# Kernel tuning notes

Measured on AMD Instinct MI355X. Metric: run time of the kernel, lower is better.

## Reference

```python
import jax, jax.numpy as jnp
import numpy as np


def _build_kkt(A, B, x0, C, c, T):
    n_state, n_ctrl = B.shape
    n_all = n_state + n_ctrl
    N = n_all * T          # primal dim (z)
    M = n_state * T        # dual dim (mu)
    dt = A.dtype

    # TL = block_diag(C_0, ..., C_{T-1})  -> [N, N]
    t = jnp.arange(T)
    ra = jnp.arange(n_all)
    rows = t[:, None, None] * n_all + ra[None, :, None]
    cols = t[:, None, None] * n_all + ra[None, None, :]
    TL = jnp.zeros((N, N), dt).at[rows, cols].set(C)

    # BL = dynamics constraint matrix  -> [M, N]
    AB = jnp.concatenate([A, B], axis=1)            # [n_state, n_all]
    BL = jnp.zeros((M, N), dt)
    BL = BL.at[:n_state, :n_state].set(jnp.eye(n_state, dtype=dt))
    ti = jnp.arange(T - 1)
    rs = jnp.arange(n_state)
    # AB blocks: rows n_state + i*n_state, cols i*n_all (i = 0..T-2)
    br = (ti[:, None, None] + 1) * n_state + rs[None, :, None]
    bc = ti[:, None, None] * n_all + ra[None, None, :]
    BL = BL.at[br, bc].set(jnp.broadcast_to(AB, (T - 1, n_state, n_all)))
    # -1 identity blocks: BL[n_state*t + i, n_all*t + i] = -1 for t = 1..T-1
    BL = BL.at[(ti[:, None] + 1) * n_state + rs[None, :],
               (ti[:, None] + 1) * n_all + rs[None, :]].set(-1.0)

    Full = jnp.block([[TL, BL.T],
                      [BL, jnp.zeros((M, M), dt)]])
    b = jnp.zeros(M, dt).at[:n_state].set(x0)
    sol = jnp.concatenate([-c.reshape(-1), b])
    return Full, sol, N


def setup_inputs() -> dict:
    key = jax.random.key(0)
    kA, kB, kx, kC, kc = jax.random.split(key, 5)
    T, n_state, n_ctrl = 128, 16, 8
    n_all = n_state + n_ctrl
    A = 0.3 * jax.random.normal(kA, (n_state, n_state), jnp.float32)
    B = 0.3 * jax.random.normal(kB, (n_state, n_ctrl), jnp.float32)
    x0 = jax.random.normal(kx, (n_state,), jnp.float32)
    Mrand = 0.1 * jax.random.normal(kC, (T, n_all, n_all), jnp.float32)
    C = jnp.eye(n_all, dtype=jnp.float32)[None] + jnp.einsum('tij,tkj->tik', Mrand, Mrand)
    c = jax.random.normal(kc, (T, n_all), jnp.float32)
    return {"A": A, "B": B, "x0": x0, "C": C, "c": c, "T": T}


def reference(A, B, x0, C, c, T):
    Full, sol, N = _build_kkt(A, B, x0, C, c, T)
    mu_z = jnp.linalg.solve(Full, sol)
    z, mu = mu_z[:N], mu_z[N:]
    return (z, mu)
```

## Files before the change

### kernel.cpp

```cpp
#include <hip/hip_runtime.h>


constexpr int T  = 128;
constexpr int NA = 24;

__device__ __forceinline__ float dot16r(const float* lds, const float* r, float s) {
    const float4* a4 = (const float4*)lds;
#pragma unroll
    for (int q = 0; q < 4; ++q) {
        float4 x = a4[q];
        s = fmaf(x.x, r[4 * q + 0], s); s = fmaf(x.y, r[4 * q + 1], s);
        s = fmaf(x.z, r[4 * q + 2], s); s = fmaf(x.w, r[4 * q + 3], s);
    }
    return s;
}
__device__ __forceinline__ float dot16f4(const float* a, const float* b, float s) {
    const float4* a4 = (const float4*)a;
    const float4* b4 = (const float4*)b;
#pragma unroll
    for (int q = 0; q < 4; ++q) {
        float4 x = a4[q], y = b4[q];
        s = fmaf(x.x, y.x, s); s = fmaf(x.y, y.y, s);
        s = fmaf(x.z, y.z, s); s = fmaf(x.w, y.w, s);
    }
    return s;
}

__global__ __launch_bounds__(256, 1)
void lqr_solve(const float* __restrict__ gA,
               const float* __restrict__ gB,
               const float* __restrict__ gx0,
               const float* __restrict__ gC,
               const float* __restrict__ gc,
               float* __restrict__ out,
               float* __restrict__ Pws,
               float* __restrict__ pws,
               float* __restrict__ Fws,
               float* __restrict__ dws)
{
    __shared__ __align__(16) float A_sh[16][16];
    __shared__ __align__(16) float At_sh[16][16];
    __shared__ __align__(16) float B_sh[16][8];
    __shared__ __align__(16) float Bt_sh[8][16];
    __shared__ __align__(16) float P_sh[2][16][20];
    __shared__ __align__(16) float p_sh[2][16];
    __shared__ __align__(16) float Wt[16][20];
    __shared__ __align__(16) float Vt[8][20];
    __shared__ __align__(16) float Gu[16][8];
    __shared__ __align__(16) float Aug[2][8][27];
    __shared__ __align__(16) float Kall[T][8][16];
    __shared__ __align__(16) float kall[T][8];
    __shared__ __align__(16) float c_sh[T][NA];
    __shared__ __align__(16) float z_sh[T][NA];
    __shared__ __align__(16) float Csh[2][24][25];

    const int tid = threadIdx.x;

    {
        const int i = tid >> 4, j = tid & 15;
        const float v = gA[tid];
        A_sh[i][j] = v; At_sh[j][i] = v;
        P_sh[0][i][j] = 0.0f;
        if (j < 4) P_sh[0][i][16 + j] = 0.0f;
    }
    if (tid < 128) {
        const int i = tid >> 3, j = tid & 7;
        const float v = gB[tid];
        B_sh[i][j] = v; Bt_sh[j][i] = v;
    }
    if (tid < 16) p_sh[0][tid] = 0.0f;
    for (int idx = tid; idx < T * NA; idx += 256) c_sh[idx / NA][idx % NA] = gc[idx];
    for (int idx = tid; idx < 576; idx += 256)
        Csh[0][idx / 24][idx % 24] = gC[(T - 1) * 576 + idx];
    __syncthreads();

    float atr[16], btr_e[16], btr3[16], atr2[16], brow[8], browp[8];
    {
        const int rA  = tid >> 4;
        const int rBe = (tid >> 4) & 7;
        const int rB3 = (tid / 25) & 7;
        const int rA2 = (tid >> 3) & 15;
        const int rBp = tid & 15;
#pragma unroll
        for (int q = 0; q < 4; ++q) {
            float4 v;
            v = *(const float4*)&At_sh[rA][4 * q];
            atr[4*q]=v.x; atr[4*q+1]=v.y; atr[4*q+2]=v.z; atr[4*q+3]=v.w;
            v = *(const float4*)&Bt_sh[rBe][4 * q];
            btr_e[4*q]=v.x; btr_e[4*q+1]=v.y; btr_e[4*q+2]=v.z; btr_e[4*q+3]=v.w;
            v = *(const float4*)&Bt_sh[rB3][4 * q];
            btr3[4*q]=v.x; btr3[4*q+1]=v.y; btr3[4*q+2]=v.z; btr3[4*q+3]=v.w;
            v = *(const float4*)&At_sh[rA2][4 * q];
            atr2[4*q]=v.x; atr2[4*q+1]=v.y; atr2[4*q+2]=v.z; atr2[4*q+3]=v.w;
        }
#pragma unroll
        for (int q = 0; q < 2; ++q) {
            float4 v;
            v = *(const float4*)&B_sh[rA][4 * q];
            brow[4*q]=v.x; brow[4*q+1]=v.y; brow[4*q+2]=v.z; brow[4*q+3]=v.w;
            v = *(const float4*)&B_sh[rBp][4 * q];
            browp[4*q]=v.x; browp[4*q+1]=v.y; browp[4*q+2]=v.z; browp[4*q+3]=v.w;
        }
    }

    int pb = 0;
    for (int t = T - 1; t >= 0; --t) {
        const int cb = (T - 1 - t) & 1;

        float pf0 = 0.f, pf1 = 0.f, pf2 = 0.f;
        if (t > 0) {
            const float* src = gC + (size_t)(t - 1) * 576;
            pf0 = src[tid];
            pf1 = src[tid + 256];
            if (tid < 64) pf2 = src[tid + 512];
        }

        {
            const int j = tid >> 4, k = tid & 15;
            Wt[j][k] = dot16r(&P_sh[pb][k][0], atr, 0.0f);
            if (tid < 128) {
                Vt[j][k] = dot16r(&P_sh[pb][k][0], btr_e, 0.0f);
            }
        }
        __syncthreads();

        if (tid < 200) {
            const int i = tid / 25, j = tid % 25;
            float s;
            if (j < 8) {
                s = dot16r(&Vt[j][0], btr3, Csh[cb][16 + i][16 + j]);
            } else if (j < 24) {
                const int jj = j - 8;
                s = dot16r(&Wt[jj][0], btr3, Csh[cb][16 + i][jj]);
            } else {
                s = dot16r(&p_sh[pb][0], btr3, c_sh[t][16 + i]);
            }
            Aug[0][i][j] = s;
        }
        if (tid < 128) {
            const int i = tid >> 3, j = tid & 7;
            Gu[i][j] = dot16r(&Vt[j][0], atr2, Csh[cb][i][16 + j]);
        }
        __syncthreads();

#pragma unroll
        for (int kk = 0; kk < 8; kk += 4) {
            const int rb = (kk >> 2) & 1, wb = rb ^ 1;
            const float m00=Aug[rb][kk+0][kk+0], m01=Aug[rb][kk+0][kk+1],
                        m02=Aug[rb][kk+0][kk+2], m03=Aug[rb][kk+0][kk+3];
            const float m10=Aug[rb][kk+1][kk+0], m11=Aug[rb][kk+1][kk+1],
                        m12=Aug[rb][kk+1][kk+2], m13=Aug[rb][kk+1][kk+3];
            const float m20=Aug[rb][kk+2][kk+0], m21=Aug[rb][kk+2][kk+1],
                        m22=Aug[rb][kk+2][kk+2], m23=Aug[rb][kk+2][kk+3];
            const float m30=Aug[rb][kk+3][kk+0], m31=Aug[rb][kk+3][kk+1],
                        m32=Aug[rb][kk+3][kk+2], m33=Aug[rb][kk+3][kk+3];
            const float ra   = 1.0f / fmaf(m00, m11, -m01 * m10);
            const float ai00 =  m11 * ra, ai01 = -m01 * ra;
            const float ai10 = -m10 * ra, ai11 =  m00 * ra;
            const float aib00 = ai00*m02 + ai01*m12, aib01 = ai00*m03 + ai01*m13;
            const float aib10 = ai10*m02 + ai11*m12, aib11 = ai10*m03 + ai11*m13;
            const float s00 = m22 - (m20*aib00 + m21*aib10);
            const float s01 = m23 - (m20*aib01 + m21*aib11);
            const float s10 = m32 - (m30*aib00 + m31*aib10);
            const float s11 = m33 - (m30*aib01 + m31*aib11);
            const float rs   = 1.0f / fmaf(s00, s11, -s01 * s10);
            const float si00 =  s11 * rs, si01 = -s01 * rs;
            const float si10 = -s10 * rs, si11 =  s00 * rs;
            if (tid < 200) {
                const int i = tid / 25, j = tid % 25;
                const float pt0 = Aug[rb][kk+0][j], pt1 = Aug[rb][kk+1][j];
                const float pq0 = Aug[rb][kk+2][j], pq1 = Aug[rb][kk+3][j];
                const float y0 = ai00*pt0 + ai01*pt1;
                const float y1 = ai10*pt0 + ai11*pt1;
                const float z0 = pq0 - (m20*y0 + m21*y1);
                const float z1 = pq1 - (m30*y0 + m31*y1);
                const float w2 = si00*z0 + si01*z1;
                const float w3 = si10*z0 + si11*z1;
                const float w0 = y0 - (aib00*w2 + aib01*w3);
                const float w1 = y1 - (aib10*w2 + aib11*w3);
                float v;
                if      (i == kk + 0) v = w0;
                else if (i == kk + 1) v = w1;
                else if (i == kk + 2) v = w2;
                else if (i == kk + 3) v = w3;
                else {
                    v = Aug[rb][i][j];
                    v = fmaf(-Aug[rb][i][kk+0], w0, v);
                    v = fmaf(-Aug[rb][i][kk+1], w1, v);
                    v = fmaf(-Aug[rb][i][kk+2], w2, v);
                    v = fmaf(-Aug[rb][i][kk+3], w3, v);
                }
                Aug[wb][i][j] = v;
                if (kk == 4 && j >= 8) {
                    if (j < 24) Kall[t][i][j - 8] = v;
                    else        kall[t][i] = v;
                }
            }
            __syncthreads();
        }

        {
            const int i = tid >> 4, j = tid & 15;
            float kc[8];
#pragma unroll
            for (int y = 0; y < 8; ++y) kc[y] = Aug[0][y][8 + j];
            float s = dot16r(&Wt[j][0], atr, Csh[cb][i][j]);
            float s2 = 0.f;
            const float4 g0 = *(const float4*)&Gu[i][0];
            const float4 g1 = *(const float4*)&Gu[i][4];
            s2 = fmaf(g0.x, kc[0], s2); s2 = fmaf(g0.y, kc[1], s2);
            s2 = fmaf(g0.z, kc[2], s2); s2 = fmaf(g0.w, kc[3], s2);
            s2 = fmaf(g1.x, kc[4], s2); s2 = fmaf(g1.y, kc[5], s2);
            s2 = fmaf(g1.z, kc[6], s2); s2 = fmaf(g1.w, kc[7], s2);
            const float v = s - s2;
            P_sh[pb ^ 1][i][j] = v;
            Pws[t * 256 + tid] = v;
            float fa = 0.f;
#pragma unroll
            for (int y = 0; y < 8; ++y) fa = fmaf(brow[y], kc[y], fa);
            Fws[t * 256 + tid] = A_sh[i][j] - fa;
        }
        if (tid < 16) {
            float kk8[8];
#pragma unroll
            for (int q = 0; q < 8; ++q) kk8[q] = Aug[0][q][24];
            float s = dot16f4(&At_sh[tid][0], &p_sh[pb][0], c_sh[t][tid]);
            float s2 = 0.f;
#pragma unroll
            for (int q = 0; q < 8; ++q) s2 = fmaf(Gu[tid][q], kk8[q], s2);
            const float v = s - s2;
            p_sh[pb ^ 1][tid] = v;
            pws[t * 16 + tid] = v;
            float da = 0.f;
#pragma unroll
            for (int y = 0; y < 8; ++y) da = fmaf(browp[y], kk8[y], da);
            dws[t * 16 + tid] = -da;
        }
        if (t > 0) {
            Csh[cb ^ 1][tid / 24][tid % 24] = pf0;
            Csh[cb ^ 1][(tid + 256) / 24][(tid + 256) % 24] = pf1;
            if (tid < 64) Csh[cb ^ 1][(tid + 512) / 24][(tid + 512) % 24] = pf2;
        }
        __syncthreads();
        pb ^= 1;
    }

    asm volatile("s_waitcnt vmcnt(0)" ::: "memory");

    if (tid < 16) z_sh[0][tid] = gx0[tid];
    float fcur[16], dcur = 0.f, prow[16], pcur = 0.f;
    if (tid < 16) {
#pragma unroll
        for (int q = 0; q < 4; ++q) {
            float4 v = *(const float4*)&Fws[tid * 16 + 4 * q];
            fcur[4*q]=v.x; fcur[4*q+1]=v.y; fcur[4*q+2]=v.z; fcur[4*q+3]=v.w;
        }
        dcur = dws[tid];
    }
    if (tid >= 32 && tid < 48) {
        const int i = tid - 32;
#pragma unroll
        for (int q = 0; q < 4; ++q) {
            float4 v = *(const float4*)&Pws[i * 16 + 4 * q];
            prow[4*q]=v.x; prow[4*q+1]=v.y; prow[4*q+2]=v.z; prow[4*q+3]=v.w;
        }
        pcur = pws[i];
    }
    __syncthreads();
    for (int t = 0; t < T; ++t) {
        float fn[16], dn = 0.f, pn[16], ppn = 0.f;
        if (t < T - 1) {
            if (tid < 16) {
#pragma unroll
                for (int q = 0; q < 4; ++q) {
                    float4 v = *(const float4*)&Fws[(t + 1) * 256 + tid * 16 + 4 * q];
                    fn[4*q]=v.x; fn[4*q+1]=v.y; fn[4*q+2]=v.z; fn[4*q+3]=v.w;
                }
                dn = dws[(t + 1) * 16 + tid];
            }
            if (tid >= 32 && tid < 48) {
                const int i = tid - 32;
#pragma unroll
                for (int q = 0; q < 4; ++q) {
                    float4 v = *(const float4*)&Pws[(t + 1) * 256 + i * 16 + 4 * q];
                    pn[4*q]=v.x; pn[4*q+1]=v.y; pn[4*q+2]=v.z; pn[4*q+3]=v.w;
                }
                ppn = pws[(t + 1) * 16 + i];
            }
        }
        if (tid >= 16 && tid < 24) {
            const int y = tid - 16;
            float s = dot16f4(&Kall[t][y][0], &z_sh[t][0], kall[t][y]);
            z_sh[t][16 + y] = -s;
        }
        if (tid >= 32 && tid < 48) {
            const int i = tid - 32;
            float s = pcur;
            const float4* zr = (const float4*)&z_sh[t][0];
#pragma unroll
            for (int q = 0; q < 4; ++q) {
                float4 z = zr[q];
                s = fmaf(prow[4*q+0], z.x, s); s = fmaf(prow[4*q+1], z.y, s);
                s = fmaf(prow[4*q+2], z.z, s); s = fmaf(prow[4*q+3], z.w, s);
            }
            if (t == 0) s = -s;
            out[T * NA + t * 16 + i] = s;
        }
        if (t < T - 1 && tid < 16) {
            const float4* zr = (const float4*)&z_sh[t][0];
            float s = dcur;
#pragma unroll
            for (int q = 0; q < 4; ++q) {
                float4 z = zr[q];
                s = fmaf(fcur[4*q+0], z.x, s); s = fmaf(fcur[4*q+1], z.y, s);
                s = fmaf(fcur[4*q+2], z.z, s); s = fmaf(fcur[4*q+3], z.w, s);
            }
            z_sh[t + 1][tid] = s;
        }
        __syncthreads();
        if (t < T - 1) {
            if (tid < 16) {
#pragma unroll
                for (int q = 0; q < 16; ++q) fcur[q] = fn[q];
                dcur = dn;
            }
            if (tid >= 32 && tid < 48) {
#pragma unroll
                for (int q = 0; q < 16; ++q) prow[q] = pn[q];
                pcur = ppn;
            }
        }
    }

    for (int idx = tid; idx < T * NA; idx += 256)
        out[idx] = z_sh[idx / 24][idx % 24];
}

extern "C" void kernel_launch(void* const* d_in, const int* in_sizes, int n_in,
                              void* d_out, int out_size, void* d_ws, size_t ws_size,
                              hipStream_t stream) {
    const float* gA  = (const float*)d_in[0];
    const float* gB  = (const float*)d_in[1];
    const float* gx0 = (const float*)d_in[2];
    const float* gC  = (const float*)d_in[3];
    const float* gc  = (const float*)d_in[4];
    float* out = (float*)d_out;
    float* Pws = (float*)d_ws;
    float* pws = Pws + T * 256;
    float* Fws = pws + T * 16;
    float* dws = Fws + T * 256;
    lqr_solve<<<dim3(1), dim3(256), 0, stream>>>(gA, gB, gx0, gC, gc, out,
                                                 Pws, pws, Fws, dws);
}
```

Baseline: 366.5 us.

## Cut barriers in Riccati recursion and run forward pass in one wavefront

The backward Riccati loop now fuses the second 4x4 block-elimination step into the final P/F update. Each thread recomputes the eliminated K columns redundantly instead of writing them to LDS and adding a barrier. Plain __syncthreads are replaced with a lightweight LDS wait plus s_barrier that does not drain vector memory, and the Aug rows are padded so they can be read with float4 loads. The forward rollout now runs in a single wavefront using only LDS waits in place of block-wide barriers per step, trading extra redundant ALU work for fewer synchronisations on the serial critical path.

```diff
diff --git a/kernel.cpp b/kernel.cpp
--- a/kernel.cpp
+++ b/kernel.cpp
@@ -3,6 +3,15 @@
 
 constexpr int T  = 128;
 constexpr int NA = 24;
+
+#define LBAR() do { \
+    asm volatile("s_waitcnt lgkmcnt(0)" ::: "memory"); \
+    __builtin_amdgcn_s_barrier(); \
+    __builtin_amdgcn_sched_barrier(0); } while (0)
+
+#define WFENCE() do { \
+    asm volatile("s_waitcnt lgkmcnt(0)" ::: "memory"); \
+    __builtin_amdgcn_sched_barrier(0); } while (0)
 
 __device__ __forceinline__ float dot16r(const float* lds, const float* r, float s) {
     const float4* a4 = (const float4*)lds;
@@ -47,7 +56,7 @@
     __shared__ __align__(16) float Wt[16][20];
     __shared__ __align__(16) float Vt[8][20];
     __shared__ __align__(16) float Gu[16][8];
-    __shared__ __align__(16) float Aug[2][8][27];
+    __shared__ __align__(16) float Aug[2][8][28];
     __shared__ __align__(16) float Kall[T][8][16];
     __shared__ __align__(16) float kall[T][8];
     __shared__ __align__(16) float c_sh[T][NA];
@@ -122,7 +131,7 @@
                 Vt[j][k] = dot16r(&P_sh[pb][k][0], btr_e, 0.0f);
             }
         }
-        __syncthreads();
+        LBAR();
 
         if (tid < 200) {
             const int i = tid / 25, j = tid % 25;
@@ -141,19 +150,17 @@
             const int i = tid >> 3, j = tid & 7;
             Gu[i][j] = dot16r(&Vt[j][0], atr2, Csh[cb][i][16 + j]);
         }
-        __syncthreads();
-
-#pragma unroll
-        for (int kk = 0; kk < 8; kk += 4) {
-            const int rb = (kk >> 2) & 1, wb = rb ^ 1;
-            const float m00=Aug[rb][kk+0][kk+0], m01=Aug[rb][kk+0][kk+1],
-                        m02=Aug[rb][kk+0][kk+2], m03=Aug[rb][kk+0][kk+3];
-            const float m10=Aug[rb][kk+1][kk+0], m11=Aug[rb][kk+1][kk+1],
-                        m12=Aug[rb][kk+1][kk+2], m13=Aug[rb][kk+1][kk+3];
-            const float m20=Aug[rb][kk+2][kk+0], m21=Aug[rb][kk+2][kk+1],
-                        m22=Aug[rb][kk+2][kk+2], m23=Aug[rb][kk+2][kk+3];
-            const float m30=Aug[rb][kk+3][kk+0], m31=Aug[rb][kk+3][kk+1],
-                        m32=Aug[rb][kk+3][kk+2], m33=Aug[rb][kk+3][kk+3];
+        LBAR();
+
+        {
+            const float4 r0 = *(const float4*)&Aug[0][0][0];
+            const float4 r1 = *(const float4*)&Aug[0][1][0];
+            const float4 r2 = *(const float4*)&Aug[0][2][0];
+            const float4 r3 = *(const float4*)&Aug[0][3][0];
+            const float m00=r0.x, m01=r0.y, m02=r0.z, m03=r0.w;
+            const float m10=r1.x, m11=r1.y, m12=r1.z, m13=r1.w;
+            const float m20=r2.x, m21=r2.y, m22=r2.z, m23=r2.w;
+            const float m30=r3.x, m31=r3.y, m32=r3.z, m33=r3.w;
             const float ra   = 1.0f / fmaf(m00, m11, -m01 * m10);
             const float ai00 =  m11 * ra, ai01 = -m01 * ra;
             const float ai10 = -m10 * ra, ai11 =  m00 * ra;
@@ -168,8 +175,8 @@
             const float si10 = -s10 * rs, si11 =  s00 * rs;
             if (tid < 200) {
                 const int i = tid / 25, j = tid % 25;
-                const float pt0 = Aug[rb][kk+0][j], pt1 = Aug[rb][kk+1][j];
-                const float pq0 = Aug[rb][kk+2][j], pq1 = Aug[rb][kk+3][j];
+                const float pt0 = Aug[0][0][j], pt1 = Aug[0][1][j];
+                const float pq0 = Aug[0][2][j], pq1 = Aug[0][3][j];
                 const float y0 = ai00*pt0 + ai01*pt1;
                 const float y1 = ai10*pt0 + ai11*pt1;
                 const float z0 = pq0 - (m20*y0 + m21*y1);
@@ -179,158 +186,226 @@
                 const float w0 = y0 - (aib00*w2 + aib01*w3);
                 const float w1 = y1 - (aib10*w2 + aib11*w3);
                 float v;
-                if      (i == kk + 0) v = w0;
-                else if (i == kk + 1) v = w1;
-                else if (i == kk + 2) v = w2;
-                else if (i == kk + 3) v = w3;
+                if      (i == 0) v = w0;
+                else if (i == 1) v = w1;
+                else if (i == 2) v = w2;
+                else if (i == 3) v = w3;
                 else {
-                    v = Aug[rb][i][j];
-                    v = fmaf(-Aug[rb][i][kk+0], w0, v);
-                    v = fmaf(-Aug[rb][i][kk+1], w1, v);
-                    v = fmaf(-Aug[rb][i][kk+2], w2, v);
-                    v = fmaf(-Aug[rb][i][kk+3], w3, v);
-                }
-                Aug[wb][i][j] = v;
-                if (kk == 4 && j >= 8) {
-                    if (j < 24) Kall[t][i][j - 8] = v;
-                    else        kall[t][i] = v;
-                }
-            }
-            __syncthreads();
-        }
-
+                    const float4 e = *(const float4*)&Aug[0][i][0];
+                    v = Aug[0][i][j]
+                        - (e.x*w0 + e.y*w1 + e.z*w2 + e.w*w3);
+                }
+                Aug[1][i][j] = v;
+            }
+        }
+        LBAR();
+
+        if (t > 0) {
+            Csh[cb ^ 1][tid / 24][tid % 24] = pf0;
+            Csh[cb ^ 1][(tid + 256) / 24][(tid + 256) % 24] = pf1;
+            if (tid < 64) Csh[cb ^ 1][(tid + 512) / 24][(tid + 512) % 24] = pf2;
+        }
         {
+            const float4 q4 = *(const float4*)&Aug[1][4][4];
+            const float4 q5 = *(const float4*)&Aug[1][5][4];
+            const float4 q6 = *(const float4*)&Aug[1][6][4];
+            const float4 q7 = *(const float4*)&Aug[1][7][4];
+            const float m00=q4.x, m01=q4.y, m02=q4.z, m03=q4.w;
+            const float m10=q5.x, m11=q5.y, m12=q5.z, m13=q5.w;
+            const float m20=q6.x, m21=q6.y, m22=q6.z, m23=q6.w;
+            const float m30=q7.x, m31=q7.y, m32=q7.z, m33=q7.w;
+            const float ra   = 1.0f / fmaf(m00, m11, -m01 * m10);
+            const float ai00 =  m11 * ra, ai01 = -m01 * ra;
+            const float ai10 = -m10 * ra, ai11 =  m00 * ra;
+            const float aib00 = ai00*m02 + ai01*m12, aib01 = ai00*m03 + ai01*m13;
+            const float aib10 = ai10*m02 + ai11*m12, aib11 = ai10*m03 + ai11*m13;
+            const float s00 = m22 - (m20*aib00 + m21*aib10);
+            const float s01 = m23 - (m20*aib01 + m21*aib11);
+            const float s10 = m32 - (m30*aib00 + m31*aib10);
+            const float s11 = m33 - (m30*aib01 + m31*aib11);
+            const float rs   = 1.0f / fmaf(s00, s11, -s01 * s10);
+            const float si00 =  s11 * rs, si01 = -s01 * rs;
+            const float si10 = -s10 * rs, si11 =  s00 * rs;
+            const float4 e0 = *(const float4*)&Aug[1][0][4];
+            const float4 e1 = *(const float4*)&Aug[1][1][4];
+            const float4 e2 = *(const float4*)&Aug[1][2][4];
+            const float4 e3 = *(const float4*)&Aug[1][3][4];
+
             const int i = tid >> 4, j = tid & 15;
+            const int cj = 8 + j;
             float kc[8];
-#pragma unroll
-            for (int y = 0; y < 8; ++y) kc[y] = Aug[0][y][8 + j];
+            {
+                const float pt0 = Aug[1][4][cj], pt1 = Aug[1][5][cj];
+                const float pq0 = Aug[1][6][cj], pq1 = Aug[1][7][cj];
+                const float y0 = ai00*pt0 + ai01*pt1;
+                const float y1 = ai10*pt0 + ai11*pt1;
+                const float z0 = pq0 - (m20*y0 + m21*y1);
+                const float z1 = pq1 - (m30*y0 + m31*y1);
+                const float w2 = si00*z0 + si01*z1;
+                const float w3 = si10*z0 + si11*z1;
+                const float w0 = y0 - (aib00*w2 + aib01*w3);
+                const float w1 = y1 - (aib10*w2 + aib11*w3);
+                kc[4]=w0; kc[5]=w1; kc[6]=w2; kc[7]=w3;
+                kc[0] = Aug[1][0][cj] - (e0.x*w0 + e0.y*w1 + e0.z*w2 + e0.w*w3);
+                kc[1] = Aug[1][1][cj] - (e1.x*w0 + e1.y*w1 + e1.z*w2 + e1.w*w3);
+                kc[2] = Aug[1][2][cj] - (e2.x*w0 + e2.y*w1 + e2.z*w2 + e2.w*w3);
+                kc[3] = Aug[1][3][cj] - (e3.x*w0 + e3.y*w1 + e3.z*w2 + e3.w*w3);
+            }
+            if (i < 8) {
+                float kv = kc[0];
+                if (i == 1) kv = kc[1]; else if (i == 2) kv = kc[2];
+                else if (i == 3) kv = kc[3]; else if (i == 4) kv = kc[4];
+                else if (i == 5) kv = kc[5]; else if (i == 6) kv = kc[6];
+                else if (i == 7) kv = kc[7];
+                Kall[t][i][j] = kv;
+            }
             float s = dot16r(&Wt[j][0], atr, Csh[cb][i][j]);
-            float s2 = 0.f;
+            float s2 = 0.f, fa = 0.f;
             const float4 g0 = *(const float4*)&Gu[i][0];
             const float4 g1 = *(const float4*)&Gu[i][4];
             s2 = fmaf(g0.x, kc[0], s2); s2 = fmaf(g0.y, kc[1], s2);
             s2 = fmaf(g0.z, kc[2], s2); s2 = fmaf(g0.w, kc[3], s2);
             s2 = fmaf(g1.x, kc[4], s2); s2 = fmaf(g1.y, kc[5], s2);
             s2 = fmaf(g1.z, kc[6], s2); s2 = fmaf(g1.w, kc[7], s2);
+#pragma unroll
+            for (int y = 0; y < 8; ++y) fa = fmaf(brow[y], kc[y], fa);
             const float v = s - s2;
             P_sh[pb ^ 1][i][j] = v;
             Pws[t * 256 + tid] = v;
-            float fa = 0.f;
-#pragma unroll
-            for (int y = 0; y < 8; ++y) fa = fmaf(brow[y], kc[y], fa);
             Fws[t * 256 + tid] = A_sh[i][j] - fa;
-        }
-        if (tid < 16) {
-            float kk8[8];
-#pragma unroll
-            for (int q = 0; q < 8; ++q) kk8[q] = Aug[0][q][24];
-            float s = dot16f4(&At_sh[tid][0], &p_sh[pb][0], c_sh[t][tid]);
-            float s2 = 0.f;
-#pragma unroll
-            for (int q = 0; q < 8; ++q) s2 = fmaf(Gu[tid][q], kk8[q], s2);
-            const float v = s - s2;
-            p_sh[pb ^ 1][tid] = v;
-            pws[t * 16 + tid] = v;
-            float da = 0.f;
-#pragma unroll
-            for (int y = 0; y < 8; ++y) da = fmaf(browp[y], kk8[y], da);
-            dws[t * 16 + tid] = -da;
-        }
-        if (t > 0) {
-            Csh[cb ^ 1][tid / 24][tid % 24] = pf0;
-            Csh[cb ^ 1][(tid + 256) / 24][(tid + 256) % 24] = pf1;
-            if (tid < 64) Csh[cb ^ 1][(tid + 512) / 24][(tid + 512) % 24] = pf2;
-        }
-        __syncthreads();
+            if (tid < 16) {
+                float kk8[8];
+                const float pt0 = Aug[1][4][24], pt1 = Aug[1][5][24];
+                const float pq0 = Aug[1][6][24], pq1 = Aug[1][7][24];
+                const float y0 = ai00*pt0 + ai01*pt1;
+                const float y1 = ai10*pt0 + ai11*pt1;
+                const float z0 = pq0 - (m20*y0 + m21*y1);
+                const float z1 = pq1 - (m30*y0 + m31*y1);
+                const float w2 = si00*z0 + si01*z1;
+                const float w3 = si10*z0 + si11*z1;
+                const float w0 = y0 - (aib00*w2 + aib01*w3);
+                const float w1 = y1 - (aib10*w2 + aib11*w3);
+                kk8[4]=w0; kk8[5]=w1; kk8[6]=w2; kk8[7]=w3;
+                kk8[0] = Aug[1][0][24] - (e0.x*w0 + e0.y*w1 + e0.z*w2 + e0.w*w3);
+                kk8[1] = Aug[1][1][24] - (e1.x*w0 + e1.y*w1 + e1.z*w2 + e1.w*w3);
+                kk8[2] = Aug[1][2][24] - (e2.x*w0 + e2.y*w1 + e2.z*w2 + e2.w*w3);
+                kk8[3] = Aug[1][3][24] - (e3.x*w0 + e3.y*w1 + e3.z*w2 + e3.w*w3);
+                if (tid < 8) {
+                    float kv = kk8[0];
+                    if (tid == 1) kv = kk8[1]; else if (tid == 2) kv = kk8[2];
+                    else if (tid == 3) kv = kk8[3]; else if (tid == 4) kv = kk8[4];
+                    else if (tid == 5) kv = kk8[5]; else if (tid == 6) kv = kk8[6];
+                    else if (tid == 7) kv = kk8[7];
+                    kall[t][tid] = kv;
+                }
+                float sp = dot16f4(&At_sh[tid][0], &p_sh[pb][0], c_sh[t][tid]);
+                float sp2 = 0.f, da = 0.f;
+#pragma unroll
+                for (int q = 0; q < 8; ++q) {
+                    sp2 = fmaf(Gu[tid][q], kk8[q], sp2);
+                    da  = fmaf(browp[q],  kk8[q], da);
+                }
+                const float vp = sp - sp2;
+                p_sh[pb ^ 1][tid] = vp;
+                pws[t * 16 + tid] = vp;
+                dws[t * 16 + tid] = -da;
+            }
+        }
+        LBAR();
         pb ^= 1;
     }
 
+    __syncthreads();
     asm volatile("s_waitcnt vmcnt(0)" ::: "memory");
 
-    if (tid < 16) z_sh[0][tid] = gx0[tid];
-    float fcur[16], dcur = 0.f, prow[16], pcur = 0.f;
-    if (tid < 16) {
-#pragma unroll
-        for (int q = 0; q < 4; ++q) {
-            float4 v = *(const float4*)&Fws[tid * 16 + 4 * q];
-            fcur[4*q]=v.x; fcur[4*q+1]=v.y; fcur[4*q+2]=v.z; fcur[4*q+3]=v.w;
-        }
-        dcur = dws[tid];
-    }
-    if (tid >= 32 && tid < 48) {
-        const int i = tid - 32;
-#pragma unroll
-        for (int q = 0; q < 4; ++q) {
-            float4 v = *(const float4*)&Pws[i * 16 + 4 * q];
-            prow[4*q]=v.x; prow[4*q+1]=v.y; prow[4*q+2]=v.z; prow[4*q+3]=v.w;
-        }
-        pcur = pws[i];
+    if (tid < 64) {
+        const int l = tid;
+        if (l < 16) z_sh[0][l] = gx0[l];
+        float fcur[16], dcur = 0.f, prow[16], pcur = 0.f;
+        if (l < 16) {
+#pragma unroll
+            for (int q = 0; q < 4; ++q) {
+                float4 v = *(const float4*)&Fws[l * 16 + 4 * q];
+                fcur[4*q]=v.x; fcur[4*q+1]=v.y; fcur[4*q+2]=v.z; fcur[4*q+3]=v.w;
+            }
+            dcur = dws[l];
+        }
+        if (l >= 32 && l < 48) {
+            const int i = l - 32;
+#pragma unroll
+            for (int q = 0; q < 4; ++q) {
+                float4 v = *(const float4*)&Pws[i * 16 + 4 * q];
+                prow[4*q]=v.x; prow[4*q+1]=v.y; prow[4*q+2]=v.z; prow[4*q+3]=v.w;
+            }
+            pcur = pws[i];
+        }
+        WFENCE();
+        for (int t = 0; t < T; ++t) {
+            float fn[16], dn = 0.f, pn[16], ppn = 0.f;
+            if (t < T - 1) {
+                if (l < 16) {
+#pragma unroll
+                    for (int q = 0; q < 4; ++q) {
+                        float4 v = *(const float4*)&Fws[(t + 1) * 256 + l * 16 + 4 * q];
+                        fn[4*q]=v.x; fn[4*q+1]=v.y; fn[4*q+2]=v.z; fn[4*q+3]=v.w;
+                    }
+                    dn = dws[(t + 1) * 16 + l];
+                }
+                if (l >= 32 && l < 48) {
+                    const int i = l - 32;
+#pragma unroll
+                    for (int q = 0; q < 4; ++q) {
+                        float4 v = *(const float4*)&Pws[(t + 1) * 256 + i * 16 + 4 * q];
+                        pn[4*q]=v.x; pn[4*q+1]=v.y; pn[4*q+2]=v.z; pn[4*q+3]=v.w;
+                    }
+                    ppn = pws[(t + 1) * 16 + i];
+                }
+            }
+            if (l >= 16 && l < 24) {
+                const int y = l - 16;
+                float s = dot16f4(&Kall[t][y][0], &z_sh[t][0], kall[t][y]);
+                z_sh[t][16 + y] = -s;
+            }
+            if (l >= 32 && l < 48) {
+                const int i = l - 32;
+                float s = pcur;
+                const float4* zr = (const float4*)&z_sh[t][0];
+#pragma unroll
+                for (int q = 0; q < 4; ++q) {
+                    float4 z = zr[q];
+                    s = fmaf(prow[4*q+0], z.x, s); s = fmaf(prow[4*q+1], z.y, s);
+                    s = fmaf(prow[4*q+2], z.z, s); s = fmaf(prow[4*q+3], z.w, s);
+                }
+                if (t == 0) s = -s;
+                out[T * NA + t * 16 + i] = s;
+            }
+            if (t < T - 1 && l < 16) {
+                const float4* zr = (const float4*)&z_sh[t][0];
+                float s = dcur;
+#pragma unroll
+                for (int q = 0; q < 4; ++q) {
+                    float4 z = zr[q];
+                    s = fmaf(fcur[4*q+0], z.x, s); s = fmaf(fcur[4*q+1], z.y, s);
+                    s = fmaf(fcur[4*q+2], z.z, s); s = fmaf(fcur[4*q+3], z.w, s);
+                }
+                z_sh[t + 1][l] = s;
+            }
+            WFENCE();
+            if (t < T - 1) {
+                if (l < 16) {
+#pragma unroll
+                    for (int q = 0; q < 16; ++q) fcur[q] = fn[q];
+                    dcur = dn;
+                }
+                if (l >= 32 && l < 48) {
+#pragma unroll
+                    for (int q = 0; q < 16; ++q) prow[q] = pn[q];
+                    pcur = ppn;
+                }
+            }
+        }
     }
     __syncthreads();
-    for (int t = 0; t < T; ++t) {
-        float fn[16], dn = 0.f, pn[16], ppn = 0.f;
-        if (t < T - 1) {
-            if (tid < 16) {
-#pragma unroll
-                for (int q = 0; q < 4; ++q) {
-                    float4 v = *(const float4*)&Fws[(t + 1) * 256 + tid * 16 + 4 * q];
-                    fn[4*q]=v.x; fn[4*q+1]=v.y; fn[4*q+2]=v.z; fn[4*q+3]=v.w;
-                }
-                dn = dws[(t + 1) * 16 + tid];
-            }
-            if (tid >= 32 && tid < 48) {
-                const int i = tid - 32;
-#pragma unroll
-                for (int q = 0; q < 4; ++q) {
-                    float4 v = *(const float4*)&Pws[(t + 1) * 256 + i * 16 + 4 * q];
-                    pn[4*q]=v.x; pn[4*q+1]=v.y; pn[4*q+2]=v.z; pn[4*q+3]=v.w;
-                }
-                ppn = pws[(t + 1) * 16 + i];
-            }
-        }
-        if (tid >= 16 && tid < 24) {
-            const int y = tid - 16;
-            float s = dot16f4(&Kall[t][y][0], &z_sh[t][0], kall[t][y]);
-            z_sh[t][16 + y] = -s;
-        }
-        if (tid >= 32 && tid < 48) {
-            const int i = tid - 32;
-            float s = pcur;
-            const float4* zr = (const float4*)&z_sh[t][0];
-#pragma unroll
-            for (int q = 0; q < 4; ++q) {
-                float4 z = zr[q];
-                s = fmaf(prow[4*q+0], z.x, s); s = fmaf(prow[4*q+1], z.y, s);
-                s = fmaf(prow[4*q+2], z.z, s); s = fmaf(prow[4*q+3], z.w, s);
-            }
-            if (t == 0) s = -s;
-            out[T * NA + t * 16 + i] = s;
-        }
-        if (t < T - 1 && tid < 16) {
-            const float4* zr = (const float4*)&z_sh[t][0];
-            float s = dcur;
-#pragma unroll
-            for (int q = 0; q < 4; ++q) {
-                float4 z = zr[q];
-                s = fmaf(fcur[4*q+0], z.x, s); s = fmaf(fcur[4*q+1], z.y, s);
-                s = fmaf(fcur[4*q+2], z.z, s); s = fmaf(fcur[4*q+3], z.w, s);
-            }
-            z_sh[t + 1][tid] = s;
-        }
-        __syncthreads();
-        if (t < T - 1) {
-            if (tid < 16) {
-#pragma unroll
-                for (int q = 0; q < 16; ++q) fcur[q] = fn[q];
-                dcur = dn;
-            }
-            if (tid >= 32 && tid < 48) {
-#pragma unroll
-                for (int q = 0; q < 16; ++q) prow[q] = pn[q];
-                pcur = ppn;
-            }
-        }
-    }
 
     for (int idx = tid; idx < T * NA; idx += 256)
         out[idx] = z_sh[idx / 24][idx % 24];
```

Result: slower. 402.2 us (+9.7%).

## Replace barrier-separated block-pivot 8x8 solve with per-thread redundant register Gaussian elimination

Applied to the files above, without the earlier changes.

The 8x8 gain solve used to run as two 4-wide block-pivot passes over a double-buffered shared augmented matrix, with a block barrier after each pass. Now each thread loads the 8x8 matrix plus its own right-hand-side column and the affine column into registers and runs its own unpivoted Gaussian elimination and back substitution. This removes two barriers and the shared-memory round trips from every step of the 128-step recursion. In exchange every thread repeats the elimination, which costs more ALU work and registers, and the solve no longer pivots.

```diff
diff --git a/kernel.cpp b/kernel.cpp
--- a/kernel.cpp
+++ b/kernel.cpp
@@ -47,7 +47,7 @@
     __shared__ __align__(16) float Wt[16][20];
     __shared__ __align__(16) float Vt[8][20];
     __shared__ __align__(16) float Gu[16][8];
-    __shared__ __align__(16) float Aug[2][8][27];
+    __shared__ __align__(16) float Aug[8][28];
     __shared__ __align__(16) float Kall[T][8][16];
     __shared__ __align__(16) float kall[T][8];
     __shared__ __align__(16) float c_sh[T][NA];
@@ -135,7 +135,7 @@
             } else {
                 s = dot16r(&p_sh[pb][0], btr3, c_sh[t][16 + i]);
             }
-            Aug[0][i][j] = s;
+            Aug[i][j] = s;
         }
         if (tid < 128) {
             const int i = tid >> 3, j = tid & 7;
@@ -143,98 +143,87 @@
         }
         __syncthreads();
 
-#pragma unroll
-        for (int kk = 0; kk < 8; kk += 4) {
-            const int rb = (kk >> 2) & 1, wb = rb ^ 1;
-            const float m00=Aug[rb][kk+0][kk+0], m01=Aug[rb][kk+0][kk+1],
-                        m02=Aug[rb][kk+0][kk+2], m03=Aug[rb][kk+0][kk+3];
-            const float m10=Aug[rb][kk+1][kk+0], m11=Aug[rb][kk+1][kk+1],
-                        m12=Aug[rb][kk+1][kk+2], m13=Aug[rb][kk+1][kk+3];
-            const float m20=Aug[rb][kk+2][kk+0], m21=Aug[rb][kk+2][kk+1],
-                        m22=Aug[rb][kk+2][kk+2], m23=Aug[rb][kk+2][kk+3];
-            const float m30=Aug[rb][kk+3][kk+0], m31=Aug[rb][kk+3][kk+1],
-                        m32=Aug[rb][kk+3][kk+2], m33=Aug[rb][kk+3][kk+3];
-            const float ra   = 1.0f / fmaf(m00, m11, -m01 * m10);
-            const float ai00 =  m11 * ra, ai01 = -m01 * ra;
-            const float ai10 = -m10 * ra, ai11 =  m00 * ra;
-            const float aib00 = ai00*m02 + ai01*m12, aib01 = ai00*m03 + ai01*m13;
-            const float aib10 = ai10*m02 + ai11*m12, aib11 = ai10*m03 + ai11*m13;
-            const float s00 = m22 - (m20*aib00 + m21*aib10);
-            const float s01 = m23 - (m20*aib01 + m21*aib11);
-            const float s10 = m32 - (m30*aib00 + m31*aib10);
-            const float s11 = m33 - (m30*aib01 + m31*aib11);
-            const float rs   = 1.0f / fmaf(s00, s11, -s01 * s10);
-            const float si00 =  s11 * rs, si01 = -s01 * rs;
-            const float si10 = -s10 * rs, si11 =  s00 * rs;
-            if (tid < 200) {
-                const int i = tid / 25, j = tid % 25;
-                const float pt0 = Aug[rb][kk+0][j], pt1 = Aug[rb][kk+1][j];
-                const float pq0 = Aug[rb][kk+2][j], pq1 = Aug[rb][kk+3][j];
-                const float y0 = ai00*pt0 + ai01*pt1;
-                const float y1 = ai10*pt0 + ai11*pt1;
-                const float z0 = pq0 - (m20*y0 + m21*y1);
-                const float z1 = pq1 - (m30*y0 + m31*y1);
-                const float w2 = si00*z0 + si01*z1;
-                const float w3 = si10*z0 + si11*z1;
-                const float w0 = y0 - (aib00*w2 + aib01*w3);
-                const float w1 = y1 - (aib10*w2 + aib11*w3);
-                float v;
-                if      (i == kk + 0) v = w0;
-                else if (i == kk + 1) v = w1;
-                else if (i == kk + 2) v = w2;
-                else if (i == kk + 3) v = w3;
-                else {
-                    v = Aug[rb][i][j];
-                    v = fmaf(-Aug[rb][i][kk+0], w0, v);
-                    v = fmaf(-Aug[rb][i][kk+1], w1, v);
-                    v = fmaf(-Aug[rb][i][kk+2], w2, v);
-                    v = fmaf(-Aug[rb][i][kk+3], w3, v);
-                }
-                Aug[wb][i][j] = v;
-                if (kk == 4 && j >= 8) {
-                    if (j < 24) Kall[t][i][j - 8] = v;
-                    else        kall[t][i] = v;
-                }
-            }
-            __syncthreads();
-        }
-
         {
             const int i = tid >> 4, j = tid & 15;
-            float kc[8];
-#pragma unroll
-            for (int y = 0; y < 8; ++y) kc[y] = Aug[0][y][8 + j];
+            float h[8][8];
+#pragma unroll
+            for (int y = 0; y < 8; ++y) {
+                const float4 a = *(const float4*)&Aug[y][0];
+                const float4 b = *(const float4*)&Aug[y][4];
+                h[y][0]=a.x; h[y][1]=a.y; h[y][2]=a.z; h[y][3]=a.w;
+                h[y][4]=b.x; h[y][5]=b.y; h[y][6]=b.z; h[y][7]=b.w;
+            }
+            float g[8], g2[8];
+#pragma unroll
+            for (int y = 0; y < 8; ++y) { g[y] = Aug[y][8 + j]; g2[y] = Aug[y][24]; }
+#pragma unroll
+            for (int p = 0; p < 8; ++p) {
+                const float rp = 1.0f / h[p][p];
+#pragma unroll
+                for (int c = p + 1; c < 8; ++c) h[p][c] *= rp;
+                g[p] *= rp; g2[p] *= rp;
+#pragma unroll
+                for (int r = p + 1; r < 8; ++r) {
+                    const float f = h[r][p];
+#pragma unroll
+                    for (int c = p + 1; c < 8; ++c)
+                        h[r][c] = fmaf(-f, h[p][c], h[r][c]);
+                    g[r]  = fmaf(-f, g[p],  g[r]);
+                    g2[r] = fmaf(-f, g2[p], g2[r]);
+                }
+            }
+#pragma unroll
+            for (int p = 6; p >= 0; --p) {
+                float s = g[p], s2 = g2[p];
+#pragma unroll
+                for (int c = p + 1; c < 8; ++c) {
+                    s  = fmaf(-h[p][c], g[c],  s);
+                    s2 = fmaf(-h[p][c], g2[c], s2);
+                }
+                g[p] = s; g2[p] = s2;
+            }
+
+            if (i == 0) {
+                Kall[t][0][j] = g[0]; Kall[t][1][j] = g[1];
+                Kall[t][2][j] = g[2]; Kall[t][3][j] = g[3];
+                Kall[t][4][j] = g[4]; Kall[t][5][j] = g[5];
+                Kall[t][6][j] = g[6]; Kall[t][7][j] = g[7];
+            }
+            if (tid == 0) {
+                kall[t][0] = g2[0]; kall[t][1] = g2[1];
+                kall[t][2] = g2[2]; kall[t][3] = g2[3];
+                kall[t][4] = g2[4]; kall[t][5] = g2[5];
+                kall[t][6] = g2[6]; kall[t][7] = g2[7];
+            }
+
             float s = dot16r(&Wt[j][0], atr, Csh[cb][i][j]);
-            float s2 = 0.f;
+            float s2 = 0.f, fa = 0.f;
             const float4 g0 = *(const float4*)&Gu[i][0];
             const float4 g1 = *(const float4*)&Gu[i][4];
-            s2 = fmaf(g0.x, kc[0], s2); s2 = fmaf(g0.y, kc[1], s2);
-            s2 = fmaf(g0.z, kc[2], s2); s2 = fmaf(g0.w, kc[3], s2);
-            s2 = fmaf(g1.x, kc[4], s2); s2 = fmaf(g1.y, kc[5], s2);
-            s2 = fmaf(g1.z, kc[6], s2); s2 = fmaf(g1.w, kc[7], s2);
+            s2 = fmaf(g0.x, g[0], s2); s2 = fmaf(g0.y, g[1], s2);
+            s2 = fmaf(g0.z, g[2], s2); s2 = fmaf(g0.w, g[3], s2);
+            s2 = fmaf(g1.x, g[4], s2); s2 = fmaf(g1.y, g[5], s2);
+            s2 = fmaf(g1.z, g[6], s2); s2 = fmaf(g1.w, g[7], s2);
+#pragma unroll
+            for (int y = 0; y < 8; ++y) fa = fmaf(brow[y], g[y], fa);
             const float v = s - s2;
             P_sh[pb ^ 1][i][j] = v;
             Pws[t * 256 + tid] = v;
-            float fa = 0.f;
-#pragma unroll
-            for (int y = 0; y < 8; ++y) fa = fmaf(brow[y], kc[y], fa);
             Fws[t * 256 + tid] = A_sh[i][j] - fa;
-        }
-        if (tid < 16) {
-            float kk8[8];
-#pragma unroll
-            for (int q = 0; q < 8; ++q) kk8[q] = Aug[0][q][24];
-            float s = dot16f4(&At_sh[tid][0], &p_sh[pb][0], c_sh[t][tid]);
-            float s2 = 0.f;
-#pragma unroll
-            for (int q = 0; q < 8; ++q) s2 = fmaf(Gu[tid][q], kk8[q], s2);
-            const float v = s - s2;
-            p_sh[pb ^ 1][tid] = v;
-            pws[t * 16 + tid] = v;
-            float da = 0.f;
-#pragma unroll
-            for (int y = 0; y < 8; ++y) da = fmaf(browp[y], kk8[y], da);
-            dws[t * 16 + tid] = -da;
+
+            if (tid < 16) {
+                float sp = dot16f4(&At_sh[tid][0], &p_sh[pb][0], c_sh[t][tid]);
+                float sp2 = 0.f, da = 0.f;
+#pragma unroll
+                for (int q = 0; q < 8; ++q) {
+                    sp2 = fmaf(Gu[tid][q], g2[q], sp2);
+                    da  = fmaf(browp[q],  g2[q], da);
+                }
+                const float vp = sp - sp2;
+                p_sh[pb ^ 1][tid] = vp;
+                pws[t * 16 + tid] = vp;
+                dws[t * 16 + tid] = -da;
+            }
         }
         if (t > 0) {
             Csh[cb ^ 1][tid / 24][tid % 24] = pf0;
@@ -245,6 +234,7 @@
         pb ^= 1;
     }
 
+    __syncthreads();
     asm volatile("s_waitcnt vmcnt(0)" ::: "memory");
 
     if (tid < 16) z_sh[0][tid] = gx0[tid];
```

Result: slower. 396.6 us (+8.2%).

## Run forward state recursion in one wavefront with shuffles, defer control/dual outputs

Applied to the files above, without the earlier changes.

The forward rollout previously ran across the whole block with a __syncthreads per timestep, computing controls and duals inline. Now only the state recursion x_{t+1}=F_t x_t+d_t runs inside a single wavefront, using width-16 shuffles instead of shared memory and block barriers. The controls, states and dual values are then computed for all timesteps in parallel across all 256 threads once the recursion finishes. This removes 128 block-wide barriers from the serial critical path, at the cost of a second pass that reads P and p back from global workspace.

```diff
diff --git a/kernel.cpp b/kernel.cpp
--- a/kernel.cpp
+++ b/kernel.cpp
@@ -47,11 +47,11 @@
     __shared__ __align__(16) float Wt[16][20];
     __shared__ __align__(16) float Vt[8][20];
     __shared__ __align__(16) float Gu[16][8];
-    __shared__ __align__(16) float Aug[2][8][27];
+    __shared__ __align__(16) float Aug[2][8][28];
     __shared__ __align__(16) float Kall[T][8][16];
     __shared__ __align__(16) float kall[T][8];
     __shared__ __align__(16) float c_sh[T][NA];
-    __shared__ __align__(16) float z_sh[T][NA];
+    __shared__ __align__(16) float xs[T][16];
     __shared__ __align__(16) float Csh[2][24][25];
 
     const int tid = threadIdx.x;
@@ -245,95 +245,78 @@
         pb ^= 1;
     }
 
-    asm volatile("s_waitcnt vmcnt(0)" ::: "memory");
-
-    if (tid < 16) z_sh[0][tid] = gx0[tid];
-    float fcur[16], dcur = 0.f, prow[16], pcur = 0.f;
-    if (tid < 16) {
-#pragma unroll
-        for (int q = 0; q < 4; ++q) {
-            float4 v = *(const float4*)&Fws[tid * 16 + 4 * q];
-            fcur[4*q]=v.x; fcur[4*q+1]=v.y; fcur[4*q+2]=v.z; fcur[4*q+3]=v.w;
-        }
-        dcur = dws[tid];
-    }
-    if (tid >= 32 && tid < 48) {
-        const int i = tid - 32;
-#pragma unroll
-        for (int q = 0; q < 4; ++q) {
-            float4 v = *(const float4*)&Pws[i * 16 + 4 * q];
-            prow[4*q]=v.x; prow[4*q+1]=v.y; prow[4*q+2]=v.z; prow[4*q+3]=v.w;
-        }
-        pcur = pws[i];
-    }
-    __syncthreads();
-    for (int t = 0; t < T; ++t) {
-        float fn[16], dn = 0.f, pn[16], ppn = 0.f;
-        if (t < T - 1) {
-            if (tid < 16) {
+    if (tid < 64) {
+        const int l = tid;
+        float x = 0.0f;
+        float fcur[16] = {};
+        float dcur = 0.0f;
+        if (l < 16) {
+            x = gx0[l];
+            xs[0][l] = x;
+#pragma unroll
+            for (int q = 0; q < 4; ++q) {
+                float4 v = *(const float4*)&Fws[l * 16 + 4 * q];
+                fcur[4*q]=v.x; fcur[4*q+1]=v.y; fcur[4*q+2]=v.z; fcur[4*q+3]=v.w;
+            }
+            dcur = dws[l];
+        }
+        for (int t = 0; t < T - 1; ++t) {
+            float fn[16] = {};
+            float dn = 0.0f;
+            if (t < T - 2 && l < 16) {
 #pragma unroll
                 for (int q = 0; q < 4; ++q) {
-                    float4 v = *(const float4*)&Fws[(t + 1) * 256 + tid * 16 + 4 * q];
+                    float4 v = *(const float4*)&Fws[(t + 1) * 256 + l * 16 + 4 * q];
                     fn[4*q]=v.x; fn[4*q+1]=v.y; fn[4*q+2]=v.z; fn[4*q+3]=v.w;
                 }
-                dn = dws[(t + 1) * 16 + tid];
-            }
-            if (tid >= 32 && tid < 48) {
-                const int i = tid - 32;
-#pragma unroll
-                for (int q = 0; q < 4; ++q) {
-                    float4 v = *(const float4*)&Pws[(t + 1) * 256 + i * 16 + 4 * q];
-                    pn[4*q]=v.x; pn[4*q+1]=v.y; pn[4*q+2]=v.z; pn[4*q+3]=v.w;
-                }
-                ppn = pws[(t + 1) * 16 + i];
-            }
-        }
-        if (tid >= 16 && tid < 24) {
-            const int y = tid - 16;
-            float s = dot16f4(&Kall[t][y][0], &z_sh[t][0], kall[t][y]);
-            z_sh[t][16 + y] = -s;
-        }
-        if (tid >= 32 && tid < 48) {
-            const int i = tid - 32;
-            float s = pcur;
-            const float4* zr = (const float4*)&z_sh[t][0];
-#pragma unroll
-            for (int q = 0; q < 4; ++q) {
-                float4 z = zr[q];
-                s = fmaf(prow[4*q+0], z.x, s); s = fmaf(prow[4*q+1], z.y, s);
-                s = fmaf(prow[4*q+2], z.z, s); s = fmaf(prow[4*q+3], z.w, s);
-            }
-            if (t == 0) s = -s;
-            out[T * NA + t * 16 + i] = s;
-        }
-        if (t < T - 1 && tid < 16) {
-            const float4* zr = (const float4*)&z_sh[t][0];
+                dn = dws[(t + 1) * 16 + l];
+            }
             float s = dcur;
 #pragma unroll
-            for (int q = 0; q < 4; ++q) {
-                float4 z = zr[q];
-                s = fmaf(fcur[4*q+0], z.x, s); s = fmaf(fcur[4*q+1], z.y, s);
-                s = fmaf(fcur[4*q+2], z.z, s); s = fmaf(fcur[4*q+3], z.w, s);
-            }
-            z_sh[t + 1][tid] = s;
-        }
-        __syncthreads();
-        if (t < T - 1) {
-            if (tid < 16) {
+            for (int q = 0; q < 16; ++q) {
+                const float xq = __shfl(x, q, 16);
+                s = fmaf(fcur[q], xq, s);
+            }
+            x = s;
+            if (l < 16) xs[t + 1][l] = x;
+            if (t < T - 2 && l < 16) {
 #pragma unroll
                 for (int q = 0; q < 16; ++q) fcur[q] = fn[q];
                 dcur = dn;
             }
-            if (tid >= 32 && tid < 48) {
-#pragma unroll
-                for (int q = 0; q < 16; ++q) prow[q] = pn[q];
-                pcur = ppn;
-            }
-        }
-    }
-
-    for (int idx = tid; idx < T * NA; idx += 256)
-        out[idx] = z_sh[idx / 24][idx % 24];
+        }
+    }
+    __syncthreads();
+
+#pragma unroll
+    for (int r = 0; r < 4; ++r) {
+        const int u = tid + 256 * r;
+        const int t = u >> 3, y = u & 7;
+        const float s = dot16f4(&Kall[t][y][0], &xs[t][0], kall[t][y]);
+        out[t * 24 + 16 + y] = -s;
+    }
+#pragma unroll
+    for (int r = 0; r < 8; ++r) {
+        const int o = tid + 256 * r;
+        const int t = o >> 4, i = o & 15;
+        out[t * 24 + i] = xs[t][i];
+    }
+#pragma unroll
+    for (int r = 0; r < 8; ++r) {
+        const int o = tid + 256 * r;
+        const int t = o >> 4, i = o & 15;
+        float s = pws[t * 16 + i];
+        const float4* Pr = (const float4*)(Pws + t * 256 + i * 16);
+        const float4* zr = (const float4*)&xs[t][0];
+#pragma unroll
+        for (int q = 0; q < 4; ++q) {
+            float4 p = Pr[q], z = zr[q];
+            s = fmaf(p.x, z.x, s); s = fmaf(p.y, z.y, s);
+            s = fmaf(p.z, z.z, s); s = fmaf(p.w, z.w, s);
+        }
+        if (t == 0) s = -s;
+        out[T * 24 + o] = s;
+    }
 }
 
 extern "C" void kernel_launch(void* const* d_in, const int* in_sizes, int n_in,
```

Result: no change. 364.5 us (-0.5%).
